# Optimization experiments

Hardware: AMD Instinct MI355X
Metric: run time of the kernel (lower is better)

The kernel has to match this reference:

```python
import jax, jax.numpy as jnp
import numpy as np

WINDOW_SIZE = 64  # matches init_kwargs


def _local_allowed_mask(L, window_size):
    # Original torch code: for query i, keys in slice [max(i-w//2,0) : min(i+w//2, L)) are allowed.
    half = window_size // 2
    i = jnp.arange(L)[:, None]
    j = jnp.arange(L)[None, :]
    return (j >= i - half) & (j < i + half)  # [L, L] bool, True = attend


def setup_inputs() -> dict:
    key = jax.random.key(0)
    kq, kk, kv = jax.random.split(key, 3)
    B, L, H, E, D = 4, 2048, 16, 64, 64
    queries = jax.random.normal(kq, (B, L, H, E), dtype=jnp.float32)
    keys = jax.random.normal(kk, (B, L, H, E), dtype=jnp.float32)
    values = jax.random.normal(kv, (B, L, H, D), dtype=jnp.float32)
    attn_mask = jnp.zeros((1,), dtype=bool)  # unused by the module
    return {"queries": queries, "keys": keys, "values": values, "attn_mask": attn_mask}


def reference(queries, keys, values, attn_mask):
    B, L, H, E = queries.shape
    scale = 1.0 / np.sqrt(E).astype(np.float32)
    allowed = _local_allowed_mask(L, WINDOW_SIZE)  # [L, L]
    # Dense scores, as in the original module (einsum 'blhe,bshe->bhls')
    scores = jnp.einsum('blhe,bshe->bhls', queries, keys)
    neg_inf = jnp.asarray(-jnp.inf, dtype=scores.dtype)
    scores = jnp.where(allowed[None, None, :, :], scores, neg_inf)
    A = jax.nn.softmax(scale * scores, axis=-1)  # [B, H, L, S]
    V = jnp.einsum('bhls,bshd->blhd', A, values)  # [B, L, H, D]
    return V
```

## Files before the change

kernel.cpp:

```cpp
#include <hip/hip_runtime.h>


#define B_ 4
#define L_ 2048
#define H_ 16
#define E_ 64
#define D_ 64

typedef __attribute__((ext_vector_type(8))) short short8;
typedef __attribute__((ext_vector_type(4))) float f32x4;

__device__ __forceinline__ unsigned int f2bf(float x) {
  unsigned int b = __float_as_uint(x);
  b += 0x7fffu + ((b >> 16) & 1u);
  return b >> 16;
}
__device__ __forceinline__ unsigned int pack2(float a, float b) {
  return f2bf(a) | (f2bf(b) << 16);
}
__device__ __forceinline__ short8 pack8(const f32x4& a, const f32x4& b) {
  union { short8 s; uint4 u; } r;
  r.u = make_uint4(pack2(a[0], a[1]), pack2(a[2], a[3]),
                   pack2(b[0], b[1]), pack2(b[2], b[3]));
  return r.s;
}
__device__ __forceinline__ int clampL(int k) {
  return k < 0 ? 0 : (k > (L_ - 1) ? (L_ - 1) : k);
}

__global__ __launch_bounds__(256, 2)
void local_attn_mfma(const float* __restrict__ qg,
                     const float* __restrict__ kg,
                     const float* __restrict__ vg,
                     float* __restrict__ og) {
  __shared__ __align__(16) float Ks32[128 * 64];
  __shared__ __align__(16) float Vs32[128 * 64];
  __shared__ __align__(16) float Qs32[64 * 64];

  const int t = threadIdx.x;
  const int q0 = blockIdx.x * 64;
  const int h = blockIdx.y;
  const int b = blockIdx.z;
  const int kstart = q0 - 32;
  const int wave = t >> 6;
  const int lane = t & 63;
  const int col16 = lane & 15;
  const int quad = lane >> 4;

  #pragma unroll
  for (int it = 0; it < 8; ++it) {
    const int cid = t + it * 256;
    const int row = cid >> 4, ch = cid & 15;
    const int chs = ch ^ (row & 15);
    const int key = clampL(kstart + row);
    const float* src = kg + ((size_t)(b * L_ + key) * H_ + h) * E_ + chs * 4;
    float* dst = &Ks32[(it * 256 + wave * 64) * 4];
    __builtin_amdgcn_global_load_lds(
        (__attribute__((address_space(1))) void*)src,
        (__attribute__((address_space(3))) void*)dst, 16, 0, 0);
  }
  #pragma unroll
  for (int it = 0; it < 8; ++it) {
    const int cid = t + it * 256;
    const int row = cid >> 4, ch = cid & 15;
    const int key = clampL(kstart + row);
    const float* src = vg + ((size_t)(b * L_ + key) * H_ + h) * D_ + ch * 4;
    float* dst = &Vs32[(it * 256 + wave * 64) * 4];
    __builtin_amdgcn_global_load_lds(
        (__attribute__((address_space(1))) void*)src,
        (__attribute__((address_space(3))) void*)dst, 16, 0, 0);
  }
  #pragma unroll
  for (int it = 0; it < 4; ++it) {
    const int cid = t + it * 256;
    const int row = cid >> 4, ch = cid & 15;
    const int chs = ch ^ (row & 15);
    const float* src = qg + ((size_t)(b * L_ + q0 + row) * H_ + h) * E_ + chs * 4;
    float* dst = &Qs32[(it * 256 + wave * 64) * 4];
    __builtin_amdgcn_global_load_lds(
        (__attribute__((address_space(1))) void*)src,
        (__attribute__((address_space(3))) void*)dst, 16, 0, 0);
  }

  __syncthreads();

  const int s0 = (2 * quad) ^ col16;
  const int s1 = (2 * quad + 1) ^ col16;
  const int s2 = (2 * quad + 8) ^ col16;
  const int s3 = (2 * quad + 9) ^ col16;

  short8 qa0, qa1;
  {
    const float* Qr = &Qs32[(wave * 16 + col16) * 64];
    qa0 = pack8(*(const f32x4*)(Qr + s0 * 4), *(const f32x4*)(Qr + s1 * 4));
    qa1 = pack8(*(const f32x4*)(Qr + s2 * 4), *(const f32x4*)(Qr + s3 * 4));
  }

  f32x4 acc[5];
  #pragma unroll
  for (int tt = 0; tt < 5; ++tt) {
    const int krow = wave * 16 + tt * 16 + col16;
    const float* Kr = &Ks32[krow * 64];
    const short8 kb0 = pack8(*(const f32x4*)(Kr + s0 * 4), *(const f32x4*)(Kr + s1 * 4));
    const short8 kb1 = pack8(*(const f32x4*)(Kr + s2 * 4), *(const f32x4*)(Kr + s3 * 4));
    f32x4 c = {0.f, 0.f, 0.f, 0.f};
    c = __builtin_amdgcn_mfma_f32_16x16x32_bf16(kb0, qa0, c, 0, 0, 0);
    c = __builtin_amdgcn_mfma_f32_16x16x32_bf16(kb1, qa1, c, 0, 0, 0);
    acc[tt] = c;
  }

  float mx = -1e30f;
  #pragma unroll
  for (int tt = 0; tt < 5; ++tt)
    #pragma unroll
    for (int r = 0; r < 4; ++r) {
      const int k_loc = tt * 16 + quad * 4 + r;
      const int gkey = kstart + wave * 16 + k_loc;
      const bool ok = ((unsigned)(k_loc - col16) < 64u) &&
                      ((unsigned)gkey < (unsigned)L_);
      const float v = ok ? acc[tt][r] * 0.125f : -1e30f;
      acc[tt][r] = v;
      mx = fmaxf(mx, v);
    }
  mx = fmaxf(mx, __shfl_xor(mx, 16));
  mx = fmaxf(mx, __shfl_xor(mx, 32));
  float s = 0.f;
  #pragma unroll
  for (int tt = 0; tt < 5; ++tt)
    #pragma unroll
    for (int r = 0; r < 4; ++r) {
      const float e = __expf(acc[tt][r] - mx);
      acc[tt][r] = e;
      s += e;
    }
  s += __shfl_xor(s, 16);
  s += __shfl_xor(s, 32);
  const float inv = 1.0f / s;

  short8 pa[3];
  {
    union { short8 s8; uint4 u4; } w;
    w.u4 = make_uint4(pack2(acc[0][0] * inv, acc[0][1] * inv),
                      pack2(acc[0][2] * inv, acc[0][3] * inv),
                      pack2(acc[1][0] * inv, acc[1][1] * inv),
                      pack2(acc[1][2] * inv, acc[1][3] * inv));
    pa[0] = w.s8;
    w.u4 = make_uint4(pack2(acc[2][0] * inv, acc[2][1] * inv),
                      pack2(acc[2][2] * inv, acc[2][3] * inv),
                      pack2(acc[3][0] * inv, acc[3][1] * inv),
                      pack2(acc[3][2] * inv, acc[3][3] * inv));
    pa[1] = w.s8;
    w.u4 = make_uint4(pack2(acc[4][0] * inv, acc[4][1] * inv),
                      pack2(acc[4][2] * inv, acc[4][3] * inv), 0u, 0u);
    pa[2] = w.s8;
  }

  f32x4 oacc[4];
  #pragma unroll
  for (int nt = 0; nt < 4; ++nt) oacc[nt] = (f32x4){0.f, 0.f, 0.f, 0.f};
  #pragma unroll
  for (int nt = 0; nt < 4; ++nt) {
    const int dim = nt * 16 + col16;
    #pragma unroll
    for (int ks = 0; ks < 3; ++ks) {
      f32x4 va, vb4;
      #pragma unroll
      for (int j = 0; j < 8; ++j) {
        int slot = wave * 16 + ks * 32 + ((j >> 2) << 4) + quad * 4 + (j & 3);
        if (ks == 2 && j >= 4) slot &= 127;
        const float vv = Vs32[slot * 64 + dim];
        if (j < 4) va[j] = vv; else vb4[j - 4] = vv;
      }
      oacc[nt] = __builtin_amdgcn_mfma_f32_16x16x32_bf16(pa[ks], pack8(va, vb4), oacc[nt], 0, 0, 0);
    }
  }

  #pragma unroll
  for (int r = 0; r < 4; ++r) {
    const int q = q0 + wave * 16 + quad * 4 + r;
    float* orow = og + ((size_t)(b * L_ + q) * H_ + h) * D_;
    #pragma unroll
    for (int nt = 0; nt < 4; ++nt)
      orow[nt * 16 + col16] = oacc[nt][r];
  }
}

extern "C" void kernel_launch(void* const* d_in, const int* in_sizes, int n_in,
                              void* d_out, int out_size, void* d_ws, size_t ws_size,
                              hipStream_t stream) {
  const float* q = (const float*)d_in[0];
  const float* k = (const float*)d_in[1];
  const float* v = (const float*)d_in[2];
  float* o = (float*)d_out;
  dim3 grid(L_ / 64, H_, B_);
  local_attn_mfma<<<grid, dim3(256), 0, stream>>>(q, k, v, o);
}
```

Measured before the change: 138.4 us.

## Process eight query tiles per block with double-buffered K/V LDS staging

Each block now walks eight consecutive 64-query tiles of one (batch, head). While the current tile is being computed, it prefetches the next tile's K/V window into a second LDS buffer via global_load_lds and loads Q straight into registers. The goal is to hide load latency behind compute and to amortize block launch. The cost is a grid 8x smaller with one 256-thread block per CU (launch bounds 1) and 128KB of LDS, which lowers occupancy. Overlapping K/V rows between adjacent tiles are still re-fetched.

Result: slower. 152.3 us (+10.0%).

```diff
diff --git a/kernel.cpp b/kernel.cpp
--- a/kernel.cpp
+++ b/kernel.cpp
@@ -6,6 +6,7 @@
 #define H_ 16
 #define E_ 64
 #define D_ 64
+#define ST 8
 
 typedef __attribute__((ext_vector_type(8))) short short8;
 typedef __attribute__((ext_vector_type(4))) float f32x4;
@@ -28,33 +29,20 @@
   return k < 0 ? 0 : (k > (L_ - 1) ? (L_ - 1) : k);
 }
 
-__global__ __launch_bounds__(256, 2)
-void local_attn_mfma(const float* __restrict__ qg,
-                     const float* __restrict__ kg,
-                     const float* __restrict__ vg,
-                     float* __restrict__ og) {
-  __shared__ __align__(16) float Ks32[128 * 64];
-  __shared__ __align__(16) float Vs32[128 * 64];
-  __shared__ __align__(16) float Qs32[64 * 64];
-
-  const int t = threadIdx.x;
-  const int q0 = blockIdx.x * 64;
-  const int h = blockIdx.y;
-  const int b = blockIdx.z;
-  const int kstart = q0 - 32;
-  const int wave = t >> 6;
-  const int lane = t & 63;
-  const int col16 = lane & 15;
-  const int quad = lane >> 4;
-
+__device__ __forceinline__ void stage_tile(const float* __restrict__ kg,
+                                           const float* __restrict__ vg,
+                                           int b, int h, int q0t,
+                                           int t, int wave,
+                                           float* Kb, float* Vb) {
+  const int kst = q0t - 32;
   #pragma unroll
   for (int it = 0; it < 8; ++it) {
     const int cid = t + it * 256;
     const int row = cid >> 4, ch = cid & 15;
     const int chs = ch ^ (row & 15);
-    const int key = clampL(kstart + row);
+    const int key = clampL(kst + row);
     const float* src = kg + ((size_t)(b * L_ + key) * H_ + h) * E_ + chs * 4;
-    float* dst = &Ks32[(it * 256 + wave * 64) * 4];
+    float* dst = Kb + (it * 256 + wave * 64) * 4;
     __builtin_amdgcn_global_load_lds(
         (__attribute__((address_space(1))) void*)src,
         (__attribute__((address_space(3))) void*)dst, 16, 0, 0);
@@ -63,125 +51,161 @@
   for (int it = 0; it < 8; ++it) {
     const int cid = t + it * 256;
     const int row = cid >> 4, ch = cid & 15;
-    const int key = clampL(kstart + row);
+    const int key = clampL(kst + row);
     const float* src = vg + ((size_t)(b * L_ + key) * H_ + h) * D_ + ch * 4;
-    float* dst = &Vs32[(it * 256 + wave * 64) * 4];
+    float* dst = Vb + (it * 256 + wave * 64) * 4;
     __builtin_amdgcn_global_load_lds(
         (__attribute__((address_space(1))) void*)src,
         (__attribute__((address_space(3))) void*)dst, 16, 0, 0);
   }
-  #pragma unroll
-  for (int it = 0; it < 4; ++it) {
-    const int cid = t + it * 256;
-    const int row = cid >> 4, ch = cid & 15;
-    const int chs = ch ^ (row & 15);
-    const float* src = qg + ((size_t)(b * L_ + q0 + row) * H_ + h) * E_ + chs * 4;
-    float* dst = &Qs32[(it * 256 + wave * 64) * 4];
-    __builtin_amdgcn_global_load_lds(
-        (__attribute__((address_space(1))) void*)src,
-        (__attribute__((address_space(3))) void*)dst, 16, 0, 0);
-  }
-
-  __syncthreads();
+}
+
+__global__ __launch_bounds__(256, 1)
+void local_attn_mfma(const float* __restrict__ qg,
+                     const float* __restrict__ kg,
+                     const float* __restrict__ vg,
+                     float* __restrict__ og) {
+  __shared__ __align__(16) float Ks32[2][128 * 64];
+  __shared__ __align__(16) float Vs32[2][128 * 64];
+
+  const int t = threadIdx.x;
+  const int tile0 = blockIdx.x * ST;
+  const int h = blockIdx.y;
+  const int b = blockIdx.z;
+  const int wave = t >> 6;
+  const int lane = t & 63;
+  const int col16 = lane & 15;
+  const int quad = lane >> 4;
 
   const int s0 = (2 * quad) ^ col16;
   const int s1 = (2 * quad + 1) ^ col16;
   const int s2 = (2 * quad + 8) ^ col16;
   const int s3 = (2 * quad + 9) ^ col16;
 
-  short8 qa0, qa1;
+  f32x4 qp0, qp1, qp2, qp3;
   {
-    const float* Qr = &Qs32[(wave * 16 + col16) * 64];
-    qa0 = pack8(*(const f32x4*)(Qr + s0 * 4), *(const f32x4*)(Qr + s1 * 4));
-    qa1 = pack8(*(const f32x4*)(Qr + s2 * 4), *(const f32x4*)(Qr + s3 * 4));
-  }
-
-  f32x4 acc[5];
-  #pragma unroll
-  for (int tt = 0; tt < 5; ++tt) {
-    const int krow = wave * 16 + tt * 16 + col16;
-    const float* Kr = &Ks32[krow * 64];
-    const short8 kb0 = pack8(*(const f32x4*)(Kr + s0 * 4), *(const f32x4*)(Kr + s1 * 4));
-    const short8 kb1 = pack8(*(const f32x4*)(Kr + s2 * 4), *(const f32x4*)(Kr + s3 * 4));
-    f32x4 c = {0.f, 0.f, 0.f, 0.f};
-    c = __builtin_amdgcn_mfma_f32_16x16x32_bf16(kb0, qa0, c, 0, 0, 0);
-    c = __builtin_amdgcn_mfma_f32_16x16x32_bf16(kb1, qa1, c, 0, 0, 0);
-    acc[tt] = c;
-  }
-
-  float mx = -1e30f;
-  #pragma unroll
-  for (int tt = 0; tt < 5; ++tt)
+    const float* pq = qg + ((size_t)(b * L_ + tile0 * 64 + wave * 16 + col16) * H_ + h) * E_ + quad * 8;
+    qp0 = *(const f32x4*)pq;
+    qp1 = *(const f32x4*)(pq + 4);
+    qp2 = *(const f32x4*)(pq + 32);
+    qp3 = *(const f32x4*)(pq + 36);
+  }
+  stage_tile(kg, vg, b, h, tile0 * 64, t, wave, &Ks32[0][0], &Vs32[0][0]);
+  short8 qa0 = pack8(qp0, qp1);
+  short8 qa1 = pack8(qp2, qp3);
+  __syncthreads();
+
+  #pragma unroll 2
+  for (int s = 0; s < ST; ++s) {
+    float* Kb = &Ks32[s & 1][0];
+    float* Vb = &Vs32[s & 1][0];
+    const int q0 = (tile0 + s) * 64;
+    const int kstart = q0 - 32;
+
+    if (s + 1 < ST) {
+      const float* pq = qg + ((size_t)(b * L_ + (q0 + 64) + wave * 16 + col16) * H_ + h) * E_ + quad * 8;
+      qp0 = *(const f32x4*)pq;
+      qp1 = *(const f32x4*)(pq + 4);
+      qp2 = *(const f32x4*)(pq + 32);
+      qp3 = *(const f32x4*)(pq + 36);
+      stage_tile(kg, vg, b, h, q0 + 64, t, wave,
+                 &Ks32[(s + 1) & 1][0], &Vs32[(s + 1) & 1][0]);
+    }
+
+    f32x4 acc[5];
+    #pragma unroll
+    for (int tt = 0; tt < 5; ++tt) {
+      const int krow = wave * 16 + tt * 16 + col16;
+      const float* Kr = Kb + krow * 64;
+      const short8 kb0 = pack8(*(const f32x4*)(Kr + s0 * 4), *(const f32x4*)(Kr + s1 * 4));
+      const short8 kb1 = pack8(*(const f32x4*)(Kr + s2 * 4), *(const f32x4*)(Kr + s3 * 4));
+      f32x4 c = {0.f, 0.f, 0.f, 0.f};
+      c = __builtin_amdgcn_mfma_f32_16x16x32_bf16(kb0, qa0, c, 0, 0, 0);
+      c = __builtin_amdgcn_mfma_f32_16x16x32_bf16(kb1, qa1, c, 0, 0, 0);
+      acc[tt] = c;
+    }
+
+    float mx = -1e30f;
+    #pragma unroll
+    for (int tt = 0; tt < 5; ++tt)
+      #pragma unroll
+      for (int r = 0; r < 4; ++r) {
+        const int k_loc = tt * 16 + quad * 4 + r;
+        const int gkey = kstart + wave * 16 + k_loc;
+        const bool ok = ((unsigned)(k_loc - col16) < 64u) &&
+                        ((unsigned)gkey < (unsigned)L_);
+        const float v = ok ? acc[tt][r] * 0.125f : -1e30f;
+        acc[tt][r] = v;
+        mx = fmaxf(mx, v);
+      }
+    mx = fmaxf(mx, __shfl_xor(mx, 16));
+    mx = fmaxf(mx, __shfl_xor(mx, 32));
+    float sum = 0.f;
+    #pragma unroll
+    for (int tt = 0; tt < 5; ++tt)
+      #pragma unroll
+      for (int r = 0; r < 4; ++r) {
+        const float e = __expf(acc[tt][r] - mx);
+        acc[tt][r] = e;
+        sum += e;
+      }
+    sum += __shfl_xor(sum, 16);
+    sum += __shfl_xor(sum, 32);
+    const float inv = 1.0f / sum;
+
+    short8 pa[3];
+    {
+      union { short8 s8; uint4 u4; } w;
+      w.u4 = make_uint4(pack2(acc[0][0] * inv, acc[0][1] * inv),
+                        pack2(acc[0][2] * inv, acc[0][3] * inv),
+                        pack2(acc[1][0] * inv, acc[1][1] * inv),
+                        pack2(acc[1][2] * inv, acc[1][3] * inv));
+      pa[0] = w.s8;
+      w.u4 = make_uint4(pack2(acc[2][0] * inv, acc[2][1] * inv),
+                        pack2(acc[2][2] * inv, acc[2][3] * inv),
+                        pack2(acc[3][0] * inv, acc[3][1] * inv),
+                        pack2(acc[3][2] * inv, acc[3][3] * inv));
+      pa[1] = w.s8;
+      w.u4 = make_uint4(pack2(acc[4][0] * inv, acc[4][1] * inv),
+                        pack2(acc[4][2] * inv, acc[4][3] * inv), 0u, 0u);
+      pa[2] = w.s8;
+    }
+
+    f32x4 oacc[4];
+    #pragma unroll
+    for (int nt = 0; nt < 4; ++nt) oacc[nt] = (f32x4){0.f, 0.f, 0.f, 0.f};
+    #pragma unroll
+    for (int nt = 0; nt < 4; ++nt) {
+      const int dim = nt * 16 + col16;
+      #pragma unroll
+      for (int ks = 0; ks < 3; ++ks) {
+        f32x4 va, vb4;
+        #pragma unroll
+        for (int j = 0; j < 8; ++j) {
+          int slot = wave * 16 + ks * 32 + ((j >> 2) << 4) + quad * 4 + (j & 3);
+          if (ks == 2 && j >= 4) slot &= 127;
+          const float vv = Vb[slot * 64 + dim];
+          if (j < 4) va[j] = vv; else vb4[j - 4] = vv;
+        }
+        oacc[nt] = __builtin_amdgcn_mfma_f32_16x16x32_bf16(pa[ks], pack8(va, vb4), oacc[nt], 0, 0, 0);
+      }
+    }
+
+    short8 qn0, qn1;
+    if (s + 1 < ST) { qn0 = pack8(qp0, qp1); qn1 = pack8(qp2, qp3); }
+
+    __syncthreads();
+
     #pragma unroll
     for (int r = 0; r < 4; ++r) {
-      const int k_loc = tt * 16 + quad * 4 + r;
-      const int gkey = kstart + wave * 16 + k_loc;
-      const bool ok = ((unsigned)(k_loc - col16) < 64u) &&
-                      ((unsigned)gkey < (unsigned)L_);
-      const float v = ok ? acc[tt][r] * 0.125f : -1e30f;
-      acc[tt][r] = v;
-      mx = fmaxf(mx, v);
-    }
-  mx = fmaxf(mx, __shfl_xor(mx, 16));
-  mx = fmaxf(mx, __shfl_xor(mx, 32));
-  float s = 0.f;
-  #pragma unroll
-  for (int tt = 0; tt < 5; ++tt)
-    #pragma unroll
-    for (int r = 0; r < 4; ++r) {
-      const float e = __expf(acc[tt][r] - mx);
-      acc[tt][r] = e;
-      s += e;
-    }
-  s += __shfl_xor(s, 16);
-  s += __shfl_xor(s, 32);
-  const float inv = 1.0f / s;
-
-  short8 pa[3];
-  {
-    union { short8 s8; uint4 u4; } w;
-    w.u4 = make_uint4(pack2(acc[0][0] * inv, acc[0][1] * inv),
-                      pack2(acc[0][2] * inv, acc[0][3] * inv),
-                      pack2(acc[1][0] * inv, acc[1][1] * inv),
-                      pack2(acc[1][2] * inv, acc[1][3] * inv));
-    pa[0] = w.s8;
-    w.u4 = make_uint4(pack2(acc[2][0] * inv, acc[2][1] * inv),
-                      pack2(acc[2][2] * inv, acc[2][3] * inv),
-                      pack2(acc[3][0] * inv, acc[3][1] * inv),
-                      pack2(acc[3][2] * inv, acc[3][3] * inv));
-    pa[1] = w.s8;
-    w.u4 = make_uint4(pack2(acc[4][0] * inv, acc[4][1] * inv),
-                      pack2(acc[4][2] * inv, acc[4][3] * inv), 0u, 0u);
-    pa[2] = w.s8;
-  }
-
-  f32x4 oacc[4];
-  #pragma unroll
-  for (int nt = 0; nt < 4; ++nt) oacc[nt] = (f32x4){0.f, 0.f, 0.f, 0.f};
-  #pragma unroll
-  for (int nt = 0; nt < 4; ++nt) {
-    const int dim = nt * 16 + col16;
-    #pragma unroll
-    for (int ks = 0; ks < 3; ++ks) {
-      f32x4 va, vb4;
-      #pragma unroll
-      for (int j = 0; j < 8; ++j) {
-        int slot = wave * 16 + ks * 32 + ((j >> 2) << 4) + quad * 4 + (j & 3);
-        if (ks == 2 && j >= 4) slot &= 127;
-        const float vv = Vs32[slot * 64 + dim];
-        if (j < 4) va[j] = vv; else vb4[j - 4] = vv;
-      }
-      oacc[nt] = __builtin_amdgcn_mfma_f32_16x16x32_bf16(pa[ks], pack8(va, vb4), oacc[nt], 0, 0, 0);
-    }
-  }
-
-  #pragma unroll
-  for (int r = 0; r < 4; ++r) {
-    const int q = q0 + wave * 16 + quad * 4 + r;
-    float* orow = og + ((size_t)(b * L_ + q) * H_ + h) * D_;
-    #pragma unroll
-    for (int nt = 0; nt < 4; ++nt)
-      orow[nt * 16 + col16] = oacc[nt][r];
+      const int q = q0 + wave * 16 + quad * 4 + r;
+      float* orow = og + ((size_t)(b * L_ + q) * H_ + h) * D_;
+      #pragma unroll
+      for (int nt = 0; nt < 4; ++nt)
+        orow[nt * 16 + col16] = oacc[nt][r];
+    }
+
+    if (s + 1 < ST) { qa0 = qn0; qa1 = qn1; }
   }
 }
 
@@ -192,6 +216,6 @@
   const float* k = (const float*)d_in[1];
   const float* v = (const float*)d_in[2];
   float* o = (float*)d_out;
-  dim3 grid(L_ / 64, H_, B_);
+  dim3 grid(L_ / (64 * ST), H_, B_);
   local_attn_mfma<<<grid, dim3(256), 0, stream>>>(q, k, v, o);
 }
```
